# Kernel tuning notes

Hardware: AMD Instinct MI355X
Metric: run time of the kernel (lower is better)

Reference implementation:

```python
import jax, jax.numpy as jnp
import numpy as np

N_CLUSTERS = 128
LATENT_NDIM = 256
ALPHA = 1.0


def setup_inputs() -> dict:
    key = jax.random.key(0)
    k1, k2 = jax.random.split(key)
    z = jax.random.normal(k1, (131072, LATENT_NDIM), dtype=jnp.float32)
    centroids = jax.random.normal(k2, (N_CLUSTERS, LATENT_NDIM), dtype=jnp.float32)
    return {"z": z, "centroids": centroids}


def _student_t(z, centroids, alpha):
    # Squared distances via expansion: ||z||^2 + ||c||^2 - 2 z @ c^T  -> [B, K]
    z_sq = jnp.sum(z * z, axis=1, keepdims=True)            # [B, 1]
    c_sq = jnp.sum(centroids * centroids, axis=1)           # [K]
    sq_dist = z_sq + c_sq[None, :] - 2.0 * (z @ centroids.T)
    norm = jnp.sqrt(jnp.maximum(sq_dist, 0.0))              # L2 norm, as in torch code
    s_tmp = (1.0 + norm / alpha) ** (-(alpha + 1.0) / 2.0)
    s = s_tmp / jnp.sum(s_tmp, axis=1, keepdims=True)
    return s


def reference(z, centroids):
    s = _student_t(z, centroids, ALPHA)
    c = jnp.argmax(s, axis=1)
    return (s, c)
```

## Files before the change

### kernel.cpp

```cpp
#include <hip/hip_runtime.h>

typedef _Float16 f16x8 __attribute__((ext_vector_type(8)));
typedef float f32x4 __attribute__((ext_vector_type(4)));
typedef unsigned int u32x4 __attribute__((ext_vector_type(4)));

#define D_DIM 256
#define K_CL  128
#define WR    16
#define MARGIN 0.1f

__device__ __forceinline__ unsigned pkf16(float a, float b) {
  return __builtin_bit_cast(unsigned, __builtin_amdgcn_cvt_pkrtz(a, b));
}

extern "C" __global__ void __launch_bounds__(64)
k_prep(const float* __restrict__ cen, unsigned int* __restrict__ bfr,
       float* __restrict__ csq_g)
{
  const int b = blockIdx.x;
  const int l = threadIdx.x;
  const int l15 = l & 15, g = l >> 4;
  const int ct = b >> 3, k = b & 7;
  const float* cp = cen + (size_t)((ct << 4) + l15) * D_DIM + (k << 5) + (g << 3);
  const float4 v0 = *(const float4*)(cp);
  const float4 v1 = *(const float4*)(cp + 4);
  *(u32x4*)((char*)bfr + (b << 10) + (l << 4)) =
      (u32x4){pkf16(v0.x, v0.y), pkf16(v0.z, v0.w),
              pkf16(v1.x, v1.y), pkf16(v1.z, v1.w)};
  if (b < 4) {
#pragma clang fp contract(off)
    float blk0 = 0.f, blk1 = 0.f;
    const int c = (b << 5) + (l >> 1), sub = l & 1;
    const float* a = cen + (size_t)c * D_DIM + (sub << 2);
#pragma unroll
    for (int b2 = 0; b2 < 2; ++b2) {
      const float* ab = a + (b2 << 7);
      const float4 w0 = *(const float4*)(ab);
      float v[4] = {w0.x * w0.x, w0.y * w0.y, w0.z * w0.z, w0.w * w0.w};
      for (int i = 1; i < 16; ++i) {
        const float4 vi = *(const float4*)(ab + (i << 3));
        v[0] = v[0] + vi.x * vi.x; v[1] = v[1] + vi.y * vi.y;
        v[2] = v[2] + vi.z * vi.z; v[3] = v[3] + vi.w * vi.w;
      }
      const float part = (v[0] + v[1]) + (v[2] + v[3]);
      if (b2 == 0) blk0 = part; else blk1 = part;
    }
    const float o0 = __shfl_xor(blk0, 1);
    const float o1 = __shfl_xor(blk1, 1);
    if (sub == 0) csq_g[c] = (blk0 + o0) + (blk1 + o1);
  }
}

extern "C" __global__ void __launch_bounds__(512)
k_main(const float* __restrict__ z, const float* __restrict__ cen,
       const unsigned int* __restrict__ bfr, const float* __restrict__ csq_g,
       float* __restrict__ s_out, float* __restrict__ c_out, int ntiles)
{
  __shared__ __align__(16) float zrow_s[8][D_DIM];
  __shared__ float stmp_s[8][K_CL];

  const int tid = threadIdx.x;
  const int w   = tid >> 6;
  const int l   = tid & 63;
  const int l15 = l & 15;
  const int g   = l >> 4;

  const int t = (blockIdx.x << 3) + w;
  if (t >= ntiles) return;
  const int row0 = t << 4;

  float csqv[8];
#pragma unroll
  for (int ct = 0; ct < 8; ++ct) csqv[ct] = csq_g[(ct << 4) + l15];

  f16x8 az[8];
  float zs = 0.f;
  const float* zr = z + (size_t)(row0 + l15) * D_DIM + (g << 3);
#pragma unroll
  for (int k = 0; k < 8; ++k) {
    const float4 v0 = *(const float4*)(zr + (k << 5));
    const float4 v1 = *(const float4*)(zr + (k << 5) + 4);
    az[k] = __builtin_bit_cast(f16x8,
        (u32x4){pkf16(v0.x, v0.y), pkf16(v0.z, v0.w),
                pkf16(v1.x, v1.y), pkf16(v1.z, v1.w)});
    zs += v0.x*v0.x + v0.y*v0.y + v0.z*v0.z + v0.w*v0.w
        + v1.x*v1.x + v1.y*v1.y + v1.z*v1.z + v1.w*v1.w;
  }
  zs += __shfl_xor(zs, 16);
  zs += __shfl_xor(zs, 32);
  float zsqj[4];
#pragma unroll
  for (int j = 0; j < 4; ++j) zsqj[j] = __shfl(zs, (g << 2) + j);

  f32x4 acc[8];
#pragma unroll
  for (int ct = 0; ct < 8; ++ct) acc[ct] = (f32x4){0.f, 0.f, 0.f, 0.f};
#pragma unroll
  for (int k = 0; k < 8; ++k) {
#pragma unroll
    for (int ct = 0; ct < 8; ++ct) {
      const f16x8 b = __builtin_bit_cast(f16x8,
          *(const u32x4*)((const char*)bfr + (((ct << 3) + k) << 10) + (l << 4)));
      acc[ct] = __builtin_amdgcn_mfma_f32_16x16x32_f16(az[k], b, acc[ct], 0, 0, 0);
    }
  }

  unsigned km1[4], km2[4];
  float rinv[4];
#pragma unroll
  for (int j = 0; j < 4; ++j) {
    unsigned m1 = 0xFFFFFFFFu, m2 = 0xFFFFFFFFu;
    float sum = 0.f;
#pragma unroll
    for (int ct = 0; ct < 8; ++ct) {
      const float sq = fmaxf(fmaf(-2.0f, acc[ct][j], zsqj[j] + csqv[ct]), 0.0f);
      const unsigned u = (__float_as_uint(sq) & 0xFFFFFF80u) | (unsigned)((ct << 4) + l15);
      const unsigned mn = min(m1, u), mx = max(m1, u);
      m1 = mn; m2 = min(m2, mx);
      sum += __builtin_amdgcn_rcpf(
          1.0f + __builtin_amdgcn_sqrtf(__uint_as_float(u & 0xFFFFFF80u)));
    }
#pragma unroll
    for (int m = 1; m <= 8; m <<= 1) {
      const unsigned o1 = __shfl_xor(m1, m);
      const unsigned o2 = __shfl_xor(m2, m);
      sum += __shfl_xor(sum, m);
      const unsigned mn = min(m1, o1), mx = max(m1, o1);
      m1 = mn; m2 = min(mx, min(m2, o2));
    }
    km1[j] = m1; km2[j] = m2;
    rinv[j] = __builtin_amdgcn_rcpf(sum);
  }

#pragma unroll
  for (int j = 0; j < 4; ++j) {
    float* srow = s_out + (size_t)(row0 + (g << 2) + j) * K_CL + l15;
#pragma unroll
    for (int ct = 0; ct < 8; ++ct) {
      const float sq = fmaxf(fmaf(-2.0f, acc[ct][j], zsqj[j] + csqv[ct]), 0.0f);
      const float sqq = __uint_as_float(__float_as_uint(sq) & 0xFFFFFF80u);
      srow[ct << 4] =
          __builtin_amdgcn_rcpf(1.0f + __builtin_amdgcn_sqrtf(sqq)) * rinv[j];
    }
    if (l15 == 0) c_out[row0 + (g << 2) + j] = (float)(km1[j] & 0x7Fu);
  }

  unsigned rowmask = 0;
#pragma unroll
  for (int j = 0; j < 4; ++j) {
    const float d1 = __uint_as_float(km1[j] & 0xFFFFFF80u);
    const float d2 = __uint_as_float(km2[j] & 0xFFFFFF80u);
    const unsigned long long b = __ballot(l15 == 0 && (d2 - d1) < MARGIN);
    rowmask |= (unsigned)(b & 1ull) << j;
    rowmask |= (unsigned)((b >> 16) & 1ull) << (4 + j);
    rowmask |= (unsigned)((b >> 32) & 1ull) << (8 + j);
    rowmask |= (unsigned)((b >> 48) & 1ull) << (12 + j);
  }

  while (rowmask) {
    const int r = __builtin_ctz(rowmask);
    rowmask &= rowmask - 1;
    const int grow = row0 + r;
    float* zrs = &zrow_s[w][0];
    float* sts = &stmp_s[w][0];
    *(float4*)(zrs + (l << 2)) =
        *(const float4*)(z + (size_t)grow * D_DIM + (l << 2));
    asm volatile("s_waitcnt lgkmcnt(0)" ::: "memory");
    float zblk = 0.f;
    if (l < 8) {
#pragma clang fp contract(off)
      float b0 = 0.f, b1 = 0.f;
      for (int b2 = 0; b2 < 2; ++b2) {
        const float* ab = zrs + (b2 << 7);
        float x = ab[l];
        float racc = x * x;
        for (int i = 1; i < 16; ++i) { x = ab[(i << 3) + l]; racc = racc + x * x; }
        racc = racc + __shfl_xor(racc, 1);
        racc = racc + __shfl_xor(racc, 2);
        racc = racc + __shfl_xor(racc, 4);
        if (b2 == 0) b0 = racc; else b1 = racc;
      }
      zblk = b0 + b1;
    }
    const float zsq_np = __shfl(zblk, 0);
    double d0 = 0.0, d1d = 0.0;
    const float* c0 = cen + (size_t)l * D_DIM;
    const float* c1 = cen + (size_t)(l + 64) * D_DIM;
    for (int d4 = 0; d4 < 64; ++d4) {
      const float4 zv = *(const float4*)(zrs + (d4 << 2));
      const float4 a0 = *(const float4*)(c0 + (d4 << 2));
      const float4 a1 = *(const float4*)(c1 + (d4 << 2));
      d0  += (double)zv.x * a0.x; d0  += (double)zv.y * a0.y;
      d0  += (double)zv.z * a0.z; d0  += (double)zv.w * a0.w;
      d1d += (double)zv.x * a1.x; d1d += (double)zv.y * a1.y;
      d1d += (double)zv.z * a1.z; d1d += (double)zv.w * a1.w;
    }
    float st0, st1;
    {
#pragma clang fp contract(off)
      const float dotf0 = (float)d0;
      const float sq0 = (zsq_np + csq_g[l]) - 2.0f * dotf0;
      st0 = 1.0f / (1.0f + sqrtf(fmaxf(sq0, 0.0f)));
      const float dotf1 = (float)d1d;
      const float sq1 = (zsq_np + csq_g[l + 64]) - 2.0f * dotf1;
      st1 = 1.0f / (1.0f + sqrtf(fmaxf(sq1, 0.0f)));
    }
    sts[l] = st0;
    sts[l + 64] = st1;
    asm volatile("s_waitcnt lgkmcnt(0)" ::: "memory");
    float sblk = 0.f;
    if (l < 8) {
#pragma clang fp contract(off)
      float racc = sts[l];
      for (int i = 1; i < 16; ++i) racc = racc + sts[(i << 3) + l];
      racc = racc + __shfl_xor(racc, 1);
      racc = racc + __shfl_xor(racc, 2);
      racc = racc + __shfl_xor(racc, 4);
      sblk = racc;
    }
    const float ssum = __shfl(sblk, 0);
    const float s0 = st0 / ssum;
    const float s1 = st1 / ssum;
    unsigned long long k0 =
        ((unsigned long long)(0x7FFFFFFFu - __float_as_uint(s0)) << 32) | (unsigned)l;
    unsigned long long k1 =
        ((unsigned long long)(0x7FFFFFFFu - __float_as_uint(s1)) << 32) | (unsigned)(l + 64);
    unsigned long long kk = k0 < k1 ? k0 : k1;
#pragma unroll
    for (int m = 1; m < 64; m <<= 1) {
      const unsigned long long o = __shfl_xor(kk, m);
      kk = o < kk ? o : kk;
    }
    if (l == 0) c_out[grow] = (float)(unsigned)(kk & 0x7Fu);
  }
}

extern "C" void kernel_launch(void* const* d_in, const int* in_sizes, int n_in,
                              void* d_out, int out_size, void* d_ws, size_t ws_size,
                              hipStream_t stream) {
  const float* z   = (const float*)d_in[0];
  const float* cen = (const float*)d_in[1];
  const int M = in_sizes[0] / D_DIM;
  float* s_out = (float*)d_out;
  float* c_out = s_out + (size_t)M * K_CL;
  const int ntiles = M / WR;

  unsigned int* bfr = (unsigned int*)d_ws;
  float* csq_g = (float*)((char*)d_ws + 65536);

  hipLaunchKernelGGL(k_prep, dim3(64), dim3(64), 0, stream, cen, bfr, csq_g);
  hipLaunchKernelGGL(k_main, dim3(ntiles / 8), dim3(512), 0, stream,
                     z, cen, bfr, csq_g, s_out, c_out, ntiles);
}
```

Before: 86.05 us.

## Process two 16-row tiles per wave to reuse centroid fragments

Each wave now handles 32 rows as two 16-row MFMA groups. Every centroid B-fragment loaded from the workspace feeds two MFMAs, halving B-operand traffic per row, and the loads are issued ahead of the MFMAs within each k step. Block size drops to 256 threads (4 waves), so the grid keeps the same row coverage. The cost is roughly doubled accumulator register use, which may lower occupancy, and fewer waves in total, which may hide memory latency less well.

```diff
diff --git a/kernel.cpp b/kernel.cpp
--- a/kernel.cpp
+++ b/kernel.cpp
@@ -6,7 +6,7 @@
 
 #define D_DIM 256
 #define K_CL  128
-#define WR    16
+#define WR    32
 #define MARGIN 0.1f
 
 __device__ __forceinline__ unsigned pkf16(float a, float b) {
@@ -51,13 +51,13 @@
   }
 }
 
-extern "C" __global__ void __launch_bounds__(512)
+extern "C" __global__ void __launch_bounds__(256)
 k_main(const float* __restrict__ z, const float* __restrict__ cen,
        const unsigned int* __restrict__ bfr, const float* __restrict__ csq_g,
        float* __restrict__ s_out, float* __restrict__ c_out, int ntiles)
 {
-  __shared__ __align__(16) float zrow_s[8][D_DIM];
-  __shared__ float stmp_s[8][K_CL];
+  __shared__ __align__(16) float zrow_s[4][D_DIM];
+  __shared__ float stmp_s[4][K_CL];
 
   const int tid = threadIdx.x;
   const int w   = tid >> 6;
@@ -65,96 +65,122 @@
   const int l15 = l & 15;
   const int g   = l >> 4;
 
-  const int t = (blockIdx.x << 3) + w;
+  const int t = (blockIdx.x << 2) + w;
   if (t >= ntiles) return;
-  const int row0 = t << 4;
+  const int row0 = t << 5;
 
   float csqv[8];
 #pragma unroll
   for (int ct = 0; ct < 8; ++ct) csqv[ct] = csq_g[(ct << 4) + l15];
 
-  f16x8 az[8];
-  float zs = 0.f;
-  const float* zr = z + (size_t)(row0 + l15) * D_DIM + (g << 3);
+  f32x4 acc[2][8];
+#pragma unroll
+  for (int gr = 0; gr < 2; ++gr)
+#pragma unroll
+    for (int ct = 0; ct < 8; ++ct) acc[gr][ct] = (f32x4){0.f, 0.f, 0.f, 0.f};
+  float zs0 = 0.f, zs1 = 0.f;
+  const float* zr0 = z + (size_t)(row0 + l15) * D_DIM + (g << 3);
+  const float* zr1 = zr0 + (size_t)16 * D_DIM;
+
 #pragma unroll
   for (int k = 0; k < 8; ++k) {
-    const float4 v0 = *(const float4*)(zr + (k << 5));
-    const float4 v1 = *(const float4*)(zr + (k << 5) + 4);
-    az[k] = __builtin_bit_cast(f16x8,
-        (u32x4){pkf16(v0.x, v0.y), pkf16(v0.z, v0.w),
-                pkf16(v1.x, v1.y), pkf16(v1.z, v1.w)});
-    zs += v0.x*v0.x + v0.y*v0.y + v0.z*v0.z + v0.w*v0.w
-        + v1.x*v1.x + v1.y*v1.y + v1.z*v1.z + v1.w*v1.w;
-  }
-  zs += __shfl_xor(zs, 16);
-  zs += __shfl_xor(zs, 32);
-  float zsqj[4];
-#pragma unroll
-  for (int j = 0; j < 4; ++j) zsqj[j] = __shfl(zs, (g << 2) + j);
-
-  f32x4 acc[8];
-#pragma unroll
-  for (int ct = 0; ct < 8; ++ct) acc[ct] = (f32x4){0.f, 0.f, 0.f, 0.f};
-#pragma unroll
-  for (int k = 0; k < 8; ++k) {
+    const float4 a0 = *(const float4*)(zr0 + (k << 5));
+    const float4 a1 = *(const float4*)(zr0 + (k << 5) + 4);
+    const float4 b0 = *(const float4*)(zr1 + (k << 5));
+    const float4 b1 = *(const float4*)(zr1 + (k << 5) + 4);
+    u32x4 bb[8];
+#pragma unroll
+    for (int ct = 0; ct < 8; ++ct)
+      bb[ct] = *(const u32x4*)((const char*)bfr + (((ct << 3) + k) << 10) + (l << 4));
+    const f16x8 az0 = __builtin_bit_cast(f16x8,
+        (u32x4){pkf16(a0.x, a0.y), pkf16(a0.z, a0.w),
+                pkf16(a1.x, a1.y), pkf16(a1.z, a1.w)});
+    const f16x8 az1 = __builtin_bit_cast(f16x8,
+        (u32x4){pkf16(b0.x, b0.y), pkf16(b0.z, b0.w),
+                pkf16(b1.x, b1.y), pkf16(b1.z, b1.w)});
+    zs0 += a0.x*a0.x + a0.y*a0.y + a0.z*a0.z + a0.w*a0.w
+         + a1.x*a1.x + a1.y*a1.y + a1.z*a1.z + a1.w*a1.w;
+    zs1 += b0.x*b0.x + b0.y*b0.y + b0.z*b0.z + b0.w*b0.w
+         + b1.x*b1.x + b1.y*b1.y + b1.z*b1.z + b1.w*b1.w;
 #pragma unroll
     for (int ct = 0; ct < 8; ++ct) {
-      const f16x8 b = __builtin_bit_cast(f16x8,
-          *(const u32x4*)((const char*)bfr + (((ct << 3) + k) << 10) + (l << 4)));
-      acc[ct] = __builtin_amdgcn_mfma_f32_16x16x32_f16(az[k], b, acc[ct], 0, 0, 0);
-    }
-  }
-
-  unsigned km1[4], km2[4];
-  float rinv[4];
+      const f16x8 bfrag = __builtin_bit_cast(f16x8, bb[ct]);
+      acc[0][ct] = __builtin_amdgcn_mfma_f32_16x16x32_f16(az0, bfrag, acc[0][ct], 0, 0, 0);
+      acc[1][ct] = __builtin_amdgcn_mfma_f32_16x16x32_f16(az1, bfrag, acc[1][ct], 0, 0, 0);
+    }
+  }
+  zs0 += __shfl_xor(zs0, 16);
+  zs0 += __shfl_xor(zs0, 32);
+  zs1 += __shfl_xor(zs1, 16);
+  zs1 += __shfl_xor(zs1, 32);
+  float zsqj[2][4];
 #pragma unroll
   for (int j = 0; j < 4; ++j) {
-    unsigned m1 = 0xFFFFFFFFu, m2 = 0xFFFFFFFFu;
-    float sum = 0.f;
-#pragma unroll
-    for (int ct = 0; ct < 8; ++ct) {
-      const float sq = fmaxf(fmaf(-2.0f, acc[ct][j], zsqj[j] + csqv[ct]), 0.0f);
-      const unsigned u = (__float_as_uint(sq) & 0xFFFFFF80u) | (unsigned)((ct << 4) + l15);
-      const unsigned mn = min(m1, u), mx = max(m1, u);
-      m1 = mn; m2 = min(m2, mx);
-      sum += __builtin_amdgcn_rcpf(
-          1.0f + __builtin_amdgcn_sqrtf(__uint_as_float(u & 0xFFFFFF80u)));
-    }
-#pragma unroll
-    for (int m = 1; m <= 8; m <<= 1) {
-      const unsigned o1 = __shfl_xor(m1, m);
-      const unsigned o2 = __shfl_xor(m2, m);
-      sum += __shfl_xor(sum, m);
-      const unsigned mn = min(m1, o1), mx = max(m1, o1);
-      m1 = mn; m2 = min(mx, min(m2, o2));
-    }
-    km1[j] = m1; km2[j] = m2;
-    rinv[j] = __builtin_amdgcn_rcpf(sum);
-  }
-
-#pragma unroll
-  for (int j = 0; j < 4; ++j) {
-    float* srow = s_out + (size_t)(row0 + (g << 2) + j) * K_CL + l15;
-#pragma unroll
-    for (int ct = 0; ct < 8; ++ct) {
-      const float sq = fmaxf(fmaf(-2.0f, acc[ct][j], zsqj[j] + csqv[ct]), 0.0f);
-      const float sqq = __uint_as_float(__float_as_uint(sq) & 0xFFFFFF80u);
-      srow[ct << 4] =
-          __builtin_amdgcn_rcpf(1.0f + __builtin_amdgcn_sqrtf(sqq)) * rinv[j];
-    }
-    if (l15 == 0) c_out[row0 + (g << 2) + j] = (float)(km1[j] & 0x7Fu);
+    zsqj[0][j] = __shfl(zs0, (g << 2) + j);
+    zsqj[1][j] = __shfl(zs1, (g << 2) + j);
+  }
+
+  unsigned km1[2][4], km2[2][4];
+  float rinv[2][4];
+#pragma unroll
+  for (int gr = 0; gr < 2; ++gr) {
+#pragma unroll
+    for (int j = 0; j < 4; ++j) {
+      unsigned m1 = 0xFFFFFFFFu, m2 = 0xFFFFFFFFu;
+      float sum = 0.f;
+#pragma unroll
+      for (int ct = 0; ct < 8; ++ct) {
+        const float sq = fmaxf(fmaf(-2.0f, acc[gr][ct][j], zsqj[gr][j] + csqv[ct]), 0.0f);
+        const unsigned u = (__float_as_uint(sq) & 0xFFFFFF80u) | (unsigned)((ct << 4) + l15);
+        const unsigned mn = min(m1, u), mx = max(m1, u);
+        m1 = mn; m2 = min(m2, mx);
+        sum += __builtin_amdgcn_rcpf(
+            1.0f + __builtin_amdgcn_sqrtf(__uint_as_float(u & 0xFFFFFF80u)));
+      }
+#pragma unroll
+      for (int m = 1; m <= 8; m <<= 1) {
+        const unsigned o1 = __shfl_xor(m1, m);
+        const unsigned o2 = __shfl_xor(m2, m);
+        sum += __shfl_xor(sum, m);
+        const unsigned mn = min(m1, o1), mx = max(m1, o1);
+        m1 = mn; m2 = min(mx, min(m2, o2));
+      }
+      km1[gr][j] = m1; km2[gr][j] = m2;
+      rinv[gr][j] = __builtin_amdgcn_rcpf(sum);
+    }
+  }
+
+#pragma unroll
+  for (int gr = 0; gr < 2; ++gr) {
+#pragma unroll
+    for (int j = 0; j < 4; ++j) {
+      const int row = row0 + (gr << 4) + (g << 2) + j;
+      float* srow = s_out + (size_t)row * K_CL + l15;
+#pragma unroll
+      for (int ct = 0; ct < 8; ++ct) {
+        const float sq = fmaxf(fmaf(-2.0f, acc[gr][ct][j], zsqj[gr][j] + csqv[ct]), 0.0f);
+        const float sqq = __uint_as_float(__float_as_uint(sq) & 0xFFFFFF80u);
+        srow[ct << 4] =
+            __builtin_amdgcn_rcpf(1.0f + __builtin_amdgcn_sqrtf(sqq)) * rinv[gr][j];
+      }
+      if (l15 == 0) c_out[row] = (float)(km1[gr][j] & 0x7Fu);
+    }
   }
 
   unsigned rowmask = 0;
 #pragma unroll
-  for (int j = 0; j < 4; ++j) {
-    const float d1 = __uint_as_float(km1[j] & 0xFFFFFF80u);
-    const float d2 = __uint_as_float(km2[j] & 0xFFFFFF80u);
-    const unsigned long long b = __ballot(l15 == 0 && (d2 - d1) < MARGIN);
-    rowmask |= (unsigned)(b & 1ull) << j;
-    rowmask |= (unsigned)((b >> 16) & 1ull) << (4 + j);
-    rowmask |= (unsigned)((b >> 32) & 1ull) << (8 + j);
-    rowmask |= (unsigned)((b >> 48) & 1ull) << (12 + j);
+  for (int gr = 0; gr < 2; ++gr) {
+#pragma unroll
+    for (int j = 0; j < 4; ++j) {
+      const float d1 = __uint_as_float(km1[gr][j] & 0xFFFFFF80u);
+      const float d2 = __uint_as_float(km2[gr][j] & 0xFFFFFF80u);
+      const unsigned long long b = __ballot(l15 == 0 && (d2 - d1) < MARGIN);
+      const int base = (gr << 4) + j;
+      rowmask |= (unsigned)(b & 1ull) << base;
+      rowmask |= (unsigned)((b >> 16) & 1ull) << (base + 4);
+      rowmask |= (unsigned)((b >> 32) & 1ull) << (base + 8);
+      rowmask |= (unsigned)((b >> 48) & 1ull) << (base + 12);
+    }
   }
 
   while (rowmask) {
@@ -249,6 +275,6 @@
   float* csq_g = (float*)((char*)d_ws + 65536);
 
   hipLaunchKernelGGL(k_prep, dim3(64), dim3(64), 0, stream, cen, bfr, csq_g);
-  hipLaunchKernelGGL(k_main, dim3(ntiles / 8), dim3(512), 0, stream,
+  hipLaunchKernelGGL(k_main, dim3(ntiles / 4), dim3(256), 0, stream,
                      z, cen, bfr, csq_g, s_out, c_out, ntiles);
 }
```

Result: slower. 109.5 us (+27.3%).
